# Performance work log

Hardware: AMD Instinct MI355X
Metric: run time of the kernel (lower is better)

## Reference

```python
import jax, jax.numpy as jnp
import numpy as np

LATENT = 64

def _linear(x, W, b):
    return x @ W.T + b

def setup_inputs() -> dict:
    key = jax.random.key(0)
    ks = jax.random.split(key, 16)
    B, D, H, L = 16384, 784, 1024, LATENT
    def u(k, shape, fan_in):
        bound = 1.0 / np.sqrt(fan_in)
        return jax.random.uniform(k, shape, jnp.float32, -bound, bound)
    inp = {
        "x": jax.random.uniform(ks[0], (B, D), jnp.float32),
        "epsilon": jax.random.normal(ks[1], (B, L), jnp.float32),
        "W_ih": u(ks[2], (H, D), D), "b_ih": u(ks[3], (H,), D),
        "W_m":  u(ks[4], (L, H), H), "b_m":  u(ks[5], (L,), H),
        "W_lv": u(ks[6], (L, H), H), "b_lv": u(ks[7], (L,), H),
        "W_ap": u(ks[8], (L, H), H), "b_ap": u(ks[9], (L,), H),
        "W_lh": u(ks[10], (H, L), L), "b_lh": u(ks[11], (H,), L),
        "W_ho": u(ks[12], (D, H), H), "b_ho": u(ks[13], (D,), H),
    }
    return inp

def reference(x, epsilon, W_ih, b_ih, W_m, b_m, W_lv, b_lv, W_ap, b_ap, W_lh, b_lh, W_ho, b_ho):
    # ----- encode -----
    hidden = jnp.tanh(_linear(x, W_ih, b_ih))            # [B,H]
    mean   = _linear(hidden, W_m, b_m)                   # [B,L]
    logvar = jnp.clip(_linear(hidden, W_lv, b_lv), -4.5, 0.0)  # Hardtanh(-4.5,0)
    approx = _linear(hidden, W_ap, b_ap)                 # [B,L]
    # ----- reparameterize (rank-1 Gaussian) -----
    # inv_cov = diag(exp(logvar)) + approx approx^T   per sample
    B, L = mean.shape
    eye = jnp.eye(L, dtype=mean.dtype)
    inv_cov = jnp.exp(logvar)[:, :, None] * eye + approx[:, :, None] * approx[:, None, :]  # [B,L,L]
    cov = jnp.linalg.inv(inv_cov)                        # batched 64x64 inverse
    # torch.potrf default returns UPPER Cholesky U with U^T U = cov -> U = chol(cov).T
    Sigma = jnp.swapaxes(jnp.linalg.cholesky(cov), -1, -2)  # [B,L,L] upper
    z = mean + jnp.einsum('bij,bj->bi', Sigma, epsilon)  # [B,L]
    # ----- decode -----
    h2 = jnp.tanh(_linear(z, W_lh, b_lh))
    x_mean = jax.nn.sigmoid(_linear(h2, W_ho, b_ho))     # [B,784]
    return (x_mean, z, mean, logvar, approx)
```

## Files before the change

### kernel.cpp

```cpp
#include <hip/hip_runtime.h>
#include <hip/hip_bf16.h>
#include <math.h>

typedef __attribute__((ext_vector_type(8))) short short8;
typedef __attribute__((ext_vector_type(4))) float f32x4;
typedef __attribute__((ext_vector_type(4))) unsigned short us4;

#define GLOBAL_AS __attribute__((address_space(1)))
#define LDS_AS __attribute__((address_space(3)))

__device__ inline void g2l16(const void* g, void* l) {
    __builtin_amdgcn_global_load_lds((const GLOBAL_AS void*)g, (LDS_AS void*)l, 16, 0, 0);
}

__device__ inline unsigned short f2bf(float f) {
    unsigned int u = __float_as_uint(f);
    return (unsigned short)((u + 0x7fffu + ((u >> 16) & 1u)) >> 16);
}

template <int EPI>
__global__ __launch_bounds__(512, 4) void mgemmB(
    const __hip_bfloat16* __restrict__ A,
    const __hip_bfloat16* __restrict__ W,
    const float* __restrict__ bias,
    void* __restrict__ outp,
    int lda, int ldb, int nT, int ldc, int Nreal)
{
    __shared__ __align__(16) __hip_bfloat16 sh[2][12288];

    const int tid  = threadIdx.x;
    const int wave = tid >> 6;
    const int lane = tid & 63;
    const int rBase = blockIdx.x * 256;
    const int cBase = blockIdx.y * 128;

    const __hip_bfloat16* Ab = A + (size_t)rBase * lda;
    const __hip_bfloat16* Wb = W + (size_t)cBase * ldb;

    const int wr = (wave >> 1) * 64;
    const int wc = (wave & 1) * 64;
    const int h  = lane >> 4;
    const int r0 = lane & 15;
    const int swz = h ^ ((r0 >> 1) & 3);

    f32x4 acc[4][4];
#pragma unroll
    for (int m = 0; m < 4; ++m)
#pragma unroll
        for (int n = 0; n < 4; ++n) acc[m][n] = (f32x4){0.f, 0.f, 0.f, 0.f};

    auto stage = [&](int bb, int t) {
        const int k0 = t * 32;
#pragma unroll
        for (int r = 0; r < 2; ++r) {
            int s2  = r * 512 + tid;
            int row = s2 >> 2;
            int cg  = (s2 & 3) ^ ((row >> 1) & 3);
            g2l16(Ab + (size_t)row * lda + k0 + cg * 8, &sh[bb][s2 * 8]);
        }
        {
            int s2  = tid;
            int row = s2 >> 2;
            int cg  = (s2 & 3) ^ ((row >> 1) & 3);
            g2l16(Wb + (size_t)row * ldb + k0 + cg * 8, &sh[bb][8192 + s2 * 8]);
        }
    };

    auto compute = [&](int bb) {
        const __hip_bfloat16* base = &sh[bb][0];
        short8 a_[4], b_[4];
#pragma unroll
        for (int m = 0; m < 4; ++m) {
            int R = wr + m * 16 + r0;
            a_[m] = *(const short8*)(base + (R * 4 + swz) * 8);
        }
#pragma unroll
        for (int n = 0; n < 4; ++n) {
            int R = wc + n * 16 + r0;
            b_[n] = *(const short8*)(base + 8192 + (R * 4 + swz) * 8);
        }
        __builtin_amdgcn_s_setprio(1);
#pragma unroll
        for (int m = 0; m < 4; ++m)
#pragma unroll
            for (int n = 0; n < 4; ++n)
                acc[m][n] = __builtin_amdgcn_mfma_f32_16x16x32_bf16(a_[m], b_[n], acc[m][n], 0, 0, 0);
        __builtin_amdgcn_s_setprio(0);
    };

    stage(0, 0);
    stage(1, 1);
    for (int t = 0; t < nT; ++t) {
        const int cur = t & 1;
        if (t + 1 < nT) asm volatile("s_waitcnt vmcnt(3)" ::: "memory");
        else            asm volatile("s_waitcnt vmcnt(0)" ::: "memory");
        __builtin_amdgcn_s_barrier();
        compute(cur);
        __builtin_amdgcn_s_barrier();
        if (t + 2 < nT) stage(cur, t + 2);
    }

    const int rq = lane >> 4;
    const int c0 = lane & 15;
#pragma unroll
    for (int m = 0; m < 4; ++m) {
#pragma unroll
        for (int n = 0; n < 4; ++n) {
            f32x4 v = acc[m][n];
            const int gc = cBase + wc + n * 16 + c0;
            const float bv = bias[gc];
#pragma unroll
            for (int j = 0; j < 4; ++j) {
                const int gr = rBase + wr + m * 16 + rq * 4 + j;
                float val = v[j] + bv;
                if (EPI == 1) {
                    ((__hip_bfloat16*)outp)[(size_t)gr * ldc + gc] = __float2bfloat16(tanhf(val));
                } else {
                    if (gc < Nreal)
                        ((float*)outp)[(size_t)gr * Nreal + gc] = 1.f / (1.f + expf(-val));
                }
            }
        }
    }
}

template <int EPI>
__global__ __launch_bounds__(256, 4) void mgemmC(
    const __hip_bfloat16* __restrict__ A,
    const __hip_bfloat16* __restrict__ W,
    const float* __restrict__ bias,
    void* __restrict__ outp,
    int lda, int ldb, int nT, int ldc, int Nreal)
{
    __shared__ __align__(16) __hip_bfloat16 sh[2][8192];

    const int tid  = threadIdx.x;
    const int wave = tid >> 6;
    const int lane = tid & 63;
    const int rBase = blockIdx.x * 128;
    const int cBase = blockIdx.y * 128;

    const __hip_bfloat16* Ab = A + (size_t)rBase * lda;
    const __hip_bfloat16* Wb = W + (size_t)cBase * ldb;

    const int wr = (wave >> 1) * 64;
    const int wc = (wave & 1) * 64;
    const int h  = lane >> 4;
    const int r0 = lane & 15;
    const int swz = h ^ ((r0 >> 1) & 3);

    f32x4 acc[4][4];
#pragma unroll
    for (int m = 0; m < 4; ++m)
#pragma unroll
        for (int n = 0; n < 4; ++n) acc[m][n] = (f32x4){0.f, 0.f, 0.f, 0.f};

    auto stage = [&](int bb, int t) {
        const int k0 = t * 32;
#pragma unroll
        for (int r = 0; r < 2; ++r) {
            int s2  = r * 256 + tid;
            int row = s2 >> 2;
            int cg  = (s2 & 3) ^ ((row >> 1) & 3);
            g2l16(Ab + (size_t)row * lda + k0 + cg * 8, &sh[bb][s2 * 8]);
            g2l16(Wb + (size_t)row * ldb + k0 + cg * 8, &sh[bb][4096 + s2 * 8]);
        }
    };

    auto compute = [&](int bb) {
        const __hip_bfloat16* base = &sh[bb][0];
        short8 a_[4], b_[4];
#pragma unroll
        for (int m = 0; m < 4; ++m) {
            int R = wr + m * 16 + r0;
            a_[m] = *(const short8*)(base + (R * 4 + swz) * 8);
        }
#pragma unroll
        for (int n = 0; n < 4; ++n) {
            int R = wc + n * 16 + r0;
            b_[n] = *(const short8*)(base + 4096 + (R * 4 + swz) * 8);
        }
        __builtin_amdgcn_s_setprio(1);
#pragma unroll
        for (int m = 0; m < 4; ++m)
#pragma unroll
            for (int n = 0; n < 4; ++n)
                acc[m][n] = __builtin_amdgcn_mfma_f32_16x16x32_bf16(a_[m], b_[n], acc[m][n], 0, 0, 0);
        __builtin_amdgcn_s_setprio(0);
    };

    stage(0, 0);
    stage(1, 1);
    for (int t = 0; t < nT; ++t) {
        const int cur = t & 1;
        if (t + 1 < nT) asm volatile("s_waitcnt vmcnt(4)" ::: "memory");
        else            asm volatile("s_waitcnt vmcnt(0)" ::: "memory");
        __builtin_amdgcn_s_barrier();
        compute(cur);
        __builtin_amdgcn_s_barrier();
        if (t + 2 < nT) stage(cur, t + 2);
    }

    const int rq = lane >> 4;
    const int c0 = lane & 15;
#pragma unroll
    for (int m = 0; m < 4; ++m) {
#pragma unroll
        for (int n = 0; n < 4; ++n) {
            f32x4 v = acc[m][n];
            const int gc = cBase + wc + n * 16 + c0;
            const float bv = bias[gc];
#pragma unroll
            for (int j = 0; j < 4; ++j) {
                const int gr = rBase + wr + m * 16 + rq * 4 + j;
                float val = v[j] + bv;
                if (EPI == 0) {
                    const int sel = gc >> 6, cc = gc & 63;
                    if (sel < 3) {
                        if (sel == 1) val = fminf(fmaxf(val, -4.5f), 0.f);
                        ((float*)outp)[(size_t)sel * (16384u * 64u) + (size_t)gr * 64 + cc] = val;
                    }
                } else if (EPI == 1) {
                    ((__hip_bfloat16*)outp)[(size_t)gr * ldc + gc] = __float2bfloat16(tanhf(val));
                }
            }
        }
    }
}

__global__ void prep1(const float* __restrict__ x, const float* __restrict__ Wih,
                      const float* __restrict__ Wm, const float* __restrict__ Wlv,
                      const float* __restrict__ Wap, const float* __restrict__ bm,
                      const float* __restrict__ blv, const float* __restrict__ bap,
                      const float* __restrict__ bho_src,
                      unsigned short* __restrict__ xw,
                      unsigned short* __restrict__ whead,
                      float* __restrict__ bhead, float* __restrict__ bho)
{
    const long SEG0 = 17408L * 208, SEG1 = SEG0 + 65536, SEG2 = SEG1 + 64, SEG3 = SEG2 + 256;
    long u = (long)blockIdx.x * 256 + threadIdx.x;
    if (u < SEG0) {
        long r = u / 208;
        int  c = (int)(u - r * 208) * 4;
        us4 o = (us4){0, 0, 0, 0};
        if (c < 784) {
            const float* src = (r < 16384) ? (x + r * 784) : (Wih + (r - 16384) * 784);
            float4 v = *(const float4*)(src + c);
            o.x = f2bf(v.x); o.y = f2bf(v.y); o.z = f2bf(v.z); o.w = f2bf(v.w);
        }
        *(us4*)(xw + r * 832 + c) = o;
    } else if (u < SEG1) {
        long t = u - SEG0;
        int r = (int)(t >> 8), c = (int)(t & 255) * 4;
        us4 o = (us4){0, 0, 0, 0};
        const float* src = nullptr;
        if (r < 64)       src = Wm + (size_t)r * 1024;
        else if (r < 128) src = Wlv + (size_t)(r - 64) * 1024;
        else if (r < 192) src = Wap + (size_t)(r - 128) * 1024;
        if (src) {
            float4 v = *(const float4*)(src + c);
            o.x = f2bf(v.x); o.y = f2bf(v.y); o.z = f2bf(v.z); o.w = f2bf(v.w);
        }
        *(us4*)(whead + (size_t)r * 1024 + c) = o;
    } else if (u < SEG2) {
        int base = (int)(u - SEG1) * 4;
#pragma unroll
        for (int k = 0; k < 4; ++k) {
            int p = base + k;
            float v = 0.f;
            if (p < 64)       v = bm[p];
            else if (p < 128) v = blv[p - 64];
            else if (p < 192) v = bap[p - 128];
            bhead[p] = v;
        }
    } else if (u < SEG3) {
        int base = (int)(u - SEG2) * 4;
#pragma unroll
        for (int k = 0; k < 4; ++k) {
            int p = base + k;
            bho[p] = (p < 784) ? bho_src[p] : 0.f;
        }
    }
}

__global__ void prep2(const float* __restrict__ Who, const float* __restrict__ Wlh,
                      unsigned short* __restrict__ whob, unsigned short* __restrict__ wlhb)
{
    const long SEG0 = 262144, SEG1 = SEG0 + 16384;
    long u = (long)blockIdx.x * 256 + threadIdx.x;
    if (u < SEG0) {
        int r = (int)(u >> 8), c = (int)(u & 255) * 4;
        us4 o = (us4){0, 0, 0, 0};
        if (r < 784) {
            float4 v = *(const float4*)(Who + (size_t)r * 1024 + c);
            o.x = f2bf(v.x); o.y = f2bf(v.y); o.z = f2bf(v.z); o.w = f2bf(v.w);
        }
        *(us4*)(whob + (size_t)r * 1024 + c) = o;
    } else if (u < SEG1) {
        long t = u - SEG0;
        int r = (int)(t >> 4), c = (int)(t & 15) * 4;
        float4 v = *(const float4*)(Wlh + (size_t)r * 64 + c);
        us4 o;
        o.x = f2bf(v.x); o.y = f2bf(v.y); o.z = f2bf(v.z); o.w = f2bf(v.w);
        *(us4*)(wlhb + (size_t)r * 64 + c) = o;
    }
}

__global__ __launch_bounds__(256) void reparam_kernel(
    const float* __restrict__ mean, const float* __restrict__ logvar,
    const float* __restrict__ approx, const float* __restrict__ eps,
    float* __restrict__ z, __hip_bfloat16* __restrict__ zb, int B)
{
    const int gid  = blockIdx.x * 256 + threadIdx.x;
    const int row  = gid >> 6;
    const int lane = threadIdx.x & 63;
    if (row >= B) return;

    const size_t idx = (size_t)row * 64 + lane;
    const float m  = mean[idx];
    const float lv = logvar[idx];
    const float a  = approx[idx];
    const float ep = eps[idx];

    const float s  = expf(-lv);
    const float x1 = a * a * s;
    const float x2 = s * a * ep;

    float R = x1, S = x2;
#pragma unroll
    for (int off = 1; off < 64; off <<= 1) {
        float r2 = __shfl_down(R, off, 64);
        float s2 = __shfl_down(S, off, 64);
        if (lane + off < 64) { R += r2; S += s2; }
    }
    const float Rexc  = R - x1;
    const float Sexc  = S - x2;
    const float inv1R = 1.f / (1.f + R);
    const float dL    = sqrtf(s * (1.f + Rexc) * inv1R);
    const float bj    = -s * a * inv1R / dL;

    const float zv = m + dL * ep + bj * Sexc;
    z[idx]  = zv;
    zb[idx] = __float2bfloat16(zv);
}

extern "C" void kernel_launch(void* const* d_in, const int* in_sizes, int n_in,
                              void* d_out, int out_size, void* d_ws, size_t ws_size,
                              hipStream_t stream)
{
    const float* x    = (const float*)d_in[0];
    const float* eps  = (const float*)d_in[1];
    const float* W_ih = (const float*)d_in[2];
    const float* b_ih = (const float*)d_in[3];
    const float* W_m  = (const float*)d_in[4];
    const float* b_m  = (const float*)d_in[5];
    const float* W_lv = (const float*)d_in[6];
    const float* b_lv = (const float*)d_in[7];
    const float* W_ap = (const float*)d_in[8];
    const float* b_ap = (const float*)d_in[9];
    const float* W_lh = (const float*)d_in[10];
    const float* b_lh = (const float*)d_in[11];
    const float* W_ho = (const float*)d_in[12];
    const float* b_ho = (const float*)d_in[13];

    const int B = 16384;

    float* out    = (float*)d_out;
    float* x_mean = out;
    float* z      = out + (size_t)B * 784;
    float* mean   = z + (size_t)B * 64;
    float* logvar = mean + (size_t)B * 64;
    float* approx = logvar + (size_t)B * 64;

    char* ws = (char*)d_ws;
    __hip_bfloat16* hb    = (__hip_bfloat16*)(ws + 0);
    __hip_bfloat16* xb    = (__hip_bfloat16*)(ws + 33554432);
    __hip_bfloat16* wihb  = (__hip_bfloat16*)(ws + 60817408);
    __hip_bfloat16* whead = (__hip_bfloat16*)(ws + 62521344);
    float*          bhead = (float*)(ws + 65273856);
    float*          bho   = (float*)(ws + 65274880);
    __hip_bfloat16* zb    = (__hip_bfloat16*)(ws + 33554432);
    __hip_bfloat16* whob  = (__hip_bfloat16*)(ws + 37748736);
    __hip_bfloat16* wlhb  = (__hip_bfloat16*)(ws + 39845888);
    __hip_bfloat16* h2b   = hb;

    {
        long total = 17408L * 208 + 65536 + 64 + 256;
        prep1<<<dim3((total + 255) / 256), dim3(256), 0, stream>>>(
            x, W_ih, W_m, W_lv, W_ap, b_m, b_lv, b_ap, b_ho,
            (unsigned short*)xb, (unsigned short*)whead, bhead, bho);
    }

    mgemmB<1><<<dim3(64, 8), dim3(512), 0, stream>>>(xb, wihb, b_ih, hb, 832, 832, 26, 1024, 1024);

    prep2<<<dim3((262144 + 16384 + 255) / 256), dim3(256), 0, stream>>>(
        W_ho, W_lh, (unsigned short*)whob, (unsigned short*)wlhb);

    mgemmC<0><<<dim3(128, 2), dim3(256), 0, stream>>>(hb, whead, bhead, mean, 1024, 1024, 32, 0, 192);

    reparam_kernel<<<dim3((B * 64) / 256), dim3(256), 0, stream>>>(mean, logvar, approx, eps, z, zb, B);

    mgemmC<1><<<dim3(128, 8), dim3(256), 0, stream>>>(zb, wlhb, b_lh, h2b, 64, 64, 2, 1024, 1024);

    mgemmB<2><<<dim3(64, 7), dim3(512), 0, stream>>>(h2b, whob, bho, x_mean, 1024, 1024, 32, 784, 784);
}
```

Measured before the change: 149.3 us.

## Fuse head GEMM with reparameterization and merge weight prep kernels

Adds a headrep kernel that computes the 192-wide head projection with MFMA and immediately applies the rank-1 reparameterization in-block, eliminating the separate head GEMM epilogue and the reparam kernel's reread of mean/logvar/approx. The two weight-conversion prep kernels are merged into one launch, and the K padding of the first GEMM is reduced from 832 to 800 to drop one K-tile. This cuts launches and global round trips, at the cost of a custom kernel with fixed tiling and changed workspace layout.

```diff
diff --git a/kernel.cpp b/kernel.cpp
--- a/kernel.cpp
+++ b/kernel.cpp
@@ -214,17 +214,148 @@
             for (int j = 0; j < 4; ++j) {
                 const int gr = rBase + wr + m * 16 + rq * 4 + j;
                 float val = v[j] + bv;
-                if (EPI == 0) {
-                    const int sel = gc >> 6, cc = gc & 63;
-                    if (sel < 3) {
-                        if (sel == 1) val = fminf(fmaxf(val, -4.5f), 0.f);
-                        ((float*)outp)[(size_t)sel * (16384u * 64u) + (size_t)gr * 64 + cc] = val;
-                    }
-                } else if (EPI == 1) {
+                if (EPI == 1) {
                     ((__hip_bfloat16*)outp)[(size_t)gr * ldc + gc] = __float2bfloat16(tanhf(val));
                 }
             }
         }
+    }
+}
+
+__global__ __launch_bounds__(256, 2) void headrep(
+    const __hip_bfloat16* __restrict__ hidden,
+    const __hip_bfloat16* __restrict__ Whead,
+    const float* __restrict__ bhead,
+    const float* __restrict__ eps,
+    float* __restrict__ meanp, float* __restrict__ logvarp,
+    float* __restrict__ approxp, float* __restrict__ zp,
+    __hip_bfloat16* __restrict__ zb)
+{
+    __shared__ __align__(16) __hip_bfloat16 sh[2][16384];
+
+    const int tid  = threadIdx.x;
+    const int wave = tid >> 6;
+    const int lane = tid & 63;
+    const int rBase = blockIdx.x * 64;
+
+    const __hip_bfloat16* Ab = hidden + (size_t)rBase * 1024;
+
+    const int wnb = wave * 48;
+    const int h  = lane >> 4;
+    const int r0 = lane & 15;
+    const int swz = h ^ ((r0 >> 1) & 3);
+
+    f32x4 acc[4][3];
+#pragma unroll
+    for (int m = 0; m < 4; ++m)
+#pragma unroll
+        for (int n = 0; n < 3; ++n) acc[m][n] = (f32x4){0.f, 0.f, 0.f, 0.f};
+
+    auto stage = [&](int bb, int t) {
+#pragma unroll
+        for (int ks = 0; ks < 2; ++ks) {
+            const int k0 = t * 64 + ks * 32;
+            {
+                int s2 = tid, row = s2 >> 2;
+                int cg = (s2 & 3) ^ ((row >> 1) & 3);
+                g2l16(Ab + (size_t)row * 1024 + k0 + cg * 8, &sh[bb][(ks * 256 + s2) * 8]);
+            }
+#pragma unroll
+            for (int r = 0; r < 3; ++r) {
+                int s2 = r * 256 + tid, row = s2 >> 2;
+                int cg = (s2 & 3) ^ ((row >> 1) & 3);
+                g2l16(Whead + (size_t)row * 1024 + k0 + cg * 8,
+                      &sh[bb][(512 + ks * 768 + s2) * 8]);
+            }
+        }
+    };
+
+    auto compute = [&](int bb) {
+#pragma unroll
+        for (int ks = 0; ks < 2; ++ks) {
+            const __hip_bfloat16* base = &sh[bb][0];
+            short8 a_[4], b_[3];
+#pragma unroll
+            for (int m = 0; m < 4; ++m) {
+                int R = m * 16 + r0;
+                a_[m] = *(const short8*)(base + ((ks * 256) + R * 4 + swz) * 8);
+            }
+#pragma unroll
+            for (int n = 0; n < 3; ++n) {
+                int R = wnb + n * 16 + r0;
+                b_[n] = *(const short8*)(base + (512 + ks * 768 + R * 4 + swz) * 8);
+            }
+            __builtin_amdgcn_s_setprio(1);
+#pragma unroll
+            for (int m = 0; m < 4; ++m)
+#pragma unroll
+                for (int n = 0; n < 3; ++n)
+                    acc[m][n] = __builtin_amdgcn_mfma_f32_16x16x32_bf16(a_[m], b_[n], acc[m][n], 0, 0, 0);
+            __builtin_amdgcn_s_setprio(0);
+        }
+    };
+
+    stage(0, 0);
+    stage(1, 1);
+    const int nT = 16;
+    for (int t = 0; t < nT; ++t) {
+        const int cur = t & 1;
+        if (t + 1 < nT) asm volatile("s_waitcnt vmcnt(8)" ::: "memory");
+        else            asm volatile("s_waitcnt vmcnt(0)" ::: "memory");
+        __builtin_amdgcn_s_barrier();
+        compute(cur);
+        __builtin_amdgcn_s_barrier();
+        if (t + 2 < nT) stage(cur, t + 2);
+    }
+
+    float* cs = (float*)&sh[0][0];
+    const int rq = lane >> 4;
+    const int c0 = lane & 15;
+#pragma unroll
+    for (int m = 0; m < 4; ++m)
+#pragma unroll
+        for (int n = 0; n < 3; ++n)
+#pragma unroll
+            for (int j = 0; j < 4; ++j)
+                cs[(m * 16 + rq * 4 + j) * 200 + wnb + n * 16 + c0] = acc[m][n][j];
+    __syncthreads();
+
+    const float bm_  = bhead[lane];
+    const float blv_ = bhead[64 + lane];
+    const float bap_ = bhead[128 + lane];
+#pragma unroll 4
+    for (int r16 = 0; r16 < 16; ++r16) {
+        const int row = wave * 16 + r16;
+        const int gr  = rBase + row;
+        const float mv = cs[row * 200 + lane] + bm_;
+        float lv = cs[row * 200 + 64 + lane] + blv_;
+        lv = fminf(fmaxf(lv, -4.5f), 0.f);
+        const float ap = cs[row * 200 + 128 + lane] + bap_;
+        const float ep = eps[(size_t)gr * 64 + lane];
+
+        const float s  = expf(-lv);
+        const float x1 = ap * ap * s;
+        const float x2 = s * ap * ep;
+        float R = x1, S = x2;
+#pragma unroll
+        for (int off = 1; off < 64; off <<= 1) {
+            float r2 = __shfl_down(R, off, 64);
+            float s2 = __shfl_down(S, off, 64);
+            if (lane + off < 64) { R += r2; S += s2; }
+        }
+        const float Rexc  = R - x1;
+        const float Sexc  = S - x2;
+        const float inv1R = 1.f / (1.f + R);
+        const float dL    = sqrtf(s * (1.f + Rexc) * inv1R);
+        const float bj    = -s * ap * inv1R / dL;
+        const float zv    = mv + dL * ep + bj * Sexc;
+
+        const size_t idx = (size_t)gr * 64 + lane;
+        meanp[idx]   = mv;
+        logvarp[idx] = lv;
+        approxp[idx] = ap;
+        zp[idx]      = zv;
+        zb[idx]      = __float2bfloat16(zv);
     }
 }
 
@@ -232,23 +363,31 @@
                       const float* __restrict__ Wm, const float* __restrict__ Wlv,
                       const float* __restrict__ Wap, const float* __restrict__ bm,
                       const float* __restrict__ blv, const float* __restrict__ bap,
+                      const float* __restrict__ Who, const float* __restrict__ Wlh,
                       const float* __restrict__ bho_src,
-                      unsigned short* __restrict__ xw,
+                      unsigned short* __restrict__ slab,
                       unsigned short* __restrict__ whead,
+                      unsigned short* __restrict__ whob,
+                      unsigned short* __restrict__ wlhb,
                       float* __restrict__ bhead, float* __restrict__ bho)
 {
-    const long SEG0 = 17408L * 208, SEG1 = SEG0 + 65536, SEG2 = SEG1 + 64, SEG3 = SEG2 + 256;
+    const long SEG0 = 17408L * 200;
+    const long SEG1 = SEG0 + 65536;
+    const long SEG2 = SEG1 + 262144;
+    const long SEG3 = SEG2 + 16384;
+    const long SEG4 = SEG3 + 64;
+    const long SEG5 = SEG4 + 256;
     long u = (long)blockIdx.x * 256 + threadIdx.x;
     if (u < SEG0) {
-        long r = u / 208;
-        int  c = (int)(u - r * 208) * 4;
+        long r = u / 200;
+        int  c = (int)(u - r * 200) * 4;
         us4 o = (us4){0, 0, 0, 0};
         if (c < 784) {
             const float* src = (r < 16384) ? (x + r * 784) : (Wih + (r - 16384) * 784);
             float4 v = *(const float4*)(src + c);
             o.x = f2bf(v.x); o.y = f2bf(v.y); o.z = f2bf(v.z); o.w = f2bf(v.w);
         }
-        *(us4*)(xw + r * 832 + c) = o;
+        *(us4*)(slab + r * 800 + c) = o;
     } else if (u < SEG1) {
         long t = u - SEG0;
         int r = (int)(t >> 8), c = (int)(t & 255) * 4;
@@ -263,7 +402,23 @@
         }
         *(us4*)(whead + (size_t)r * 1024 + c) = o;
     } else if (u < SEG2) {
-        int base = (int)(u - SEG1) * 4;
+        long t = u - SEG1;
+        int r = (int)(t >> 8), c = (int)(t & 255) * 4;
+        us4 o = (us4){0, 0, 0, 0};
+        if (r < 784) {
+            float4 v = *(const float4*)(Who + (size_t)r * 1024 + c);
+            o.x = f2bf(v.x); o.y = f2bf(v.y); o.z = f2bf(v.z); o.w = f2bf(v.w);
+        }
+        *(us4*)(whob + (size_t)r * 1024 + c) = o;
+    } else if (u < SEG3) {
+        long t = u - SEG2;
+        int r = (int)(t >> 4), c = (int)(t & 15) * 4;
+        float4 v = *(const float4*)(Wlh + (size_t)r * 64 + c);
+        us4 o;
+        o.x = f2bf(v.x); o.y = f2bf(v.y); o.z = f2bf(v.z); o.w = f2bf(v.w);
+        *(us4*)(wlhb + (size_t)r * 64 + c) = o;
+    } else if (u < SEG4) {
+        int base = (int)(u - SEG3) * 4;
 #pragma unroll
         for (int k = 0; k < 4; ++k) {
             int p = base + k;
@@ -273,75 +428,14 @@
             else if (p < 192) v = bap[p - 128];
             bhead[p] = v;
         }
-    } else if (u < SEG3) {
-        int base = (int)(u - SEG2) * 4;
+    } else if (u < SEG5) {
+        int base = (int)(u - SEG4) * 4;
 #pragma unroll
         for (int k = 0; k < 4; ++k) {
             int p = base + k;
             bho[p] = (p < 784) ? bho_src[p] : 0.f;
         }
     }
-}
-
-__global__ void prep2(const float* __restrict__ Who, const float* __restrict__ Wlh,
-                      unsigned short* __restrict__ whob, unsigned short* __restrict__ wlhb)
-{
-    const long SEG0 = 262144, SEG1 = SEG0 + 16384;
-    long u = (long)blockIdx.x * 256 + threadIdx.x;
-    if (u < SEG0) {
-        int r = (int)(u >> 8), c = (int)(u & 255) * 4;
-        us4 o = (us4){0, 0, 0, 0};
-        if (r < 784) {
-            float4 v = *(const float4*)(Who + (size_t)r * 1024 + c);
-            o.x = f2bf(v.x); o.y = f2bf(v.y); o.z = f2bf(v.z); o.w = f2bf(v.w);
-        }
-        *(us4*)(whob + (size_t)r * 1024 + c) = o;
-    } else if (u < SEG1) {
-        long t = u - SEG0;
-        int r = (int)(t >> 4), c = (int)(t & 15) * 4;
-        float4 v = *(const float4*)(Wlh + (size_t)r * 64 + c);
-        us4 o;
-        o.x = f2bf(v.x); o.y = f2bf(v.y); o.z = f2bf(v.z); o.w = f2bf(v.w);
-        *(us4*)(wlhb + (size_t)r * 64 + c) = o;
-    }
-}
-
-__global__ __launch_bounds__(256) void reparam_kernel(
-    const float* __restrict__ mean, const float* __restrict__ logvar,
-    const float* __restrict__ approx, const float* __restrict__ eps,
-    float* __restrict__ z, __hip_bfloat16* __restrict__ zb, int B)
-{
-    const int gid  = blockIdx.x * 256 + threadIdx.x;
-    const int row  = gid >> 6;
-    const int lane = threadIdx.x & 63;
-    if (row >= B) return;
-
-    const size_t idx = (size_t)row * 64 + lane;
-    const float m  = mean[idx];
-    const float lv = logvar[idx];
-    const float a  = approx[idx];
-    const float ep = eps[idx];
-
-    const float s  = expf(-lv);
-    const float x1 = a * a * s;
-    const float x2 = s * a * ep;
-
-    float R = x1, S = x2;
-#pragma unroll
-    for (int off = 1; off < 64; off <<= 1) {
-        float r2 = __shfl_down(R, off, 64);
-        float s2 = __shfl_down(S, off, 64);
-        if (lane + off < 64) { R += r2; S += s2; }
-    }
-    const float Rexc  = R - x1;
-    const float Sexc  = S - x2;
-    const float inv1R = 1.f / (1.f + R);
-    const float dL    = sqrtf(s * (1.f + Rexc) * inv1R);
-    const float bj    = -s * a * inv1R / dL;
-
-    const float zv = m + dL * ep + bj * Sexc;
-    z[idx]  = zv;
-    zb[idx] = __float2bfloat16(zv);
 }
 
 extern "C" void kernel_launch(void* const* d_in, const int* in_sizes, int n_in,
@@ -375,30 +469,27 @@
     char* ws = (char*)d_ws;
     __hip_bfloat16* hb    = (__hip_bfloat16*)(ws + 0);
     __hip_bfloat16* xb    = (__hip_bfloat16*)(ws + 33554432);
-    __hip_bfloat16* wihb  = (__hip_bfloat16*)(ws + 60817408);
-    __hip_bfloat16* whead = (__hip_bfloat16*)(ws + 62521344);
-    float*          bhead = (float*)(ws + 65273856);
-    float*          bho   = (float*)(ws + 65274880);
+    __hip_bfloat16* wihb  = (__hip_bfloat16*)(ws + 33554432 + 16384L * 800 * 2);
+    __hip_bfloat16* whead = (__hip_bfloat16*)(ws + 61407232);
+    __hip_bfloat16* whob  = (__hip_bfloat16*)(ws + 61931520);
+    __hip_bfloat16* wlhb  = (__hip_bfloat16*)(ws + 64028672);
+    float*          bhead = (float*)(ws + 64159744);
+    float*          bho   = (float*)(ws + 64160768);
     __hip_bfloat16* zb    = (__hip_bfloat16*)(ws + 33554432);
-    __hip_bfloat16* whob  = (__hip_bfloat16*)(ws + 37748736);
-    __hip_bfloat16* wlhb  = (__hip_bfloat16*)(ws + 39845888);
     __hip_bfloat16* h2b   = hb;
 
     {
-        long total = 17408L * 208 + 65536 + 64 + 256;
+        long total = 17408L * 200 + 65536 + 262144 + 16384 + 64 + 256;
         prep1<<<dim3((total + 255) / 256), dim3(256), 0, stream>>>(
-            x, W_ih, W_m, W_lv, W_ap, b_m, b_lv, b_ap, b_ho,
-            (unsigned short*)xb, (unsigned short*)whead, bhead, bho);
-    }
-
-    mgemmB<1><<<dim3(64, 8), dim3(512), 0, stream>>>(xb, wihb, b_ih, hb, 832, 832, 26, 1024, 1024);
-
-    prep2<<<dim3((262144 + 16384 + 255) / 256), dim3(256), 0, stream>>>(
-        W_ho, W_lh, (unsigned short*)whob, (unsigned short*)wlhb);
-
-    mgemmC<0><<<dim3(128, 2), dim3(256), 0, stream>>>(hb, whead, bhead, mean, 1024, 1024, 32, 0, 192);
-
-    reparam_kernel<<<dim3((B * 64) / 256), dim3(256), 0, stream>>>(mean, logvar, approx, eps, z, zb, B);
+            x, W_ih, W_m, W_lv, W_ap, b_m, b_lv, b_ap, W_ho, W_lh, b_ho,
+            (unsigned short*)xb, (unsigned short*)whead, (unsigned short*)whob,
+            (unsigned short*)wlhb, bhead, bho);
+    }
+
+    mgemmB<1><<<dim3(64, 8), dim3(512), 0, stream>>>(xb, wihb, b_ih, hb, 800, 800, 25, 1024, 1024);
+
+    headrep<<<dim3(256), dim3(256), 0, stream>>>(hb, whead, bhead, eps,
+                                                 mean, logvar, approx, z, zb);
 
     mgemmC<1><<<dim3(128, 8), dim3(256), 0, stream>>>(zb, wlhb, b_lh, h2b, 64, 64, 2, 1024, 1024);
 
```

New measurement: 144.9 us (median of 2 runs). 3.0% less time.
